# Optimization experiments

Measured on AMD Instinct MI355X. Metric: run time of the kernel, lower is better.

The kernel has to match this reference:

```python
import jax, jax.numpy as jnp
import numpy as np

B, S, E, H = 2, 2048, 1024, 16
D = E // H  # head_dim = 64
MASKED_BIAS = -10000.0


def setup_inputs() -> dict:
    key = jax.random.key(0)
    k1, k2, k3 = jax.random.split(key, 3)
    return {
        "hidden_states": jax.random.normal(k1, (B, S, E), dtype=jnp.float32),
        "w_attn": jax.random.normal(k2, (E, 3 * E), dtype=jnp.float32) * 0.02,
        "b_attn": jnp.zeros((3 * E,), dtype=jnp.float32),
        "w_proj": jax.random.normal(k3, (E, E), dtype=jnp.float32) * 0.02,
        "b_proj": jnp.zeros((E,), dtype=jnp.float32),
    }


def reference(hidden_states, w_attn, b_attn, w_proj, b_proj):
    # c_attn: [B,S,E] @ [E,3E] + bias
    qkv = hidden_states @ w_attn + b_attn
    q, k, v = jnp.split(qkv, 3, axis=-1)

    def split_heads(t):  # [B,S,E] -> [B,H,S,D]
        return t.reshape(B, S, H, D).transpose(0, 2, 1, 3)

    q, k, v = split_heads(q), split_heads(k), split_heads(v)

    # scores: [B,H,S,S], scaled by sqrt(head_dim)
    scores = jnp.einsum("bhqd,bhkd->bhqk", q, k) / jnp.float32(D) ** 0.5
    causal = jnp.tril(jnp.ones((S, S), dtype=bool))
    scores = jnp.where(causal, scores, jnp.float32(MASKED_BIAS))
    attn_weights = jax.nn.softmax(scores, axis=-1)
    # dropout p=0 (eval): identity
    attn_out = jnp.einsum("bhqk,bhkd->bhqd", attn_weights, v)
    # merge heads: [B,H,S,D] -> [B,S,E]
    attn_out = attn_out.transpose(0, 2, 1, 3).reshape(B, S, E)
    attn_out = attn_out @ w_proj + b_proj
    return attn_out, attn_weights
```

## Files before the change

kernel.cpp:

```cpp
#include <hip/hip_runtime.h>


typedef unsigned short u16;
typedef __attribute__((ext_vector_type(8))) short bf16x8;
typedef __attribute__((ext_vector_type(4))) float f32x4;
typedef __attribute__((ext_vector_type(4))) unsigned short u16x4;

#define MFMA(a, b, c) __builtin_amdgcn_mfma_f32_16x16x32_bf16((a), (b), (c), 0, 0, 0)

typedef const __attribute__((address_space(1))) void* gas_t;
typedef __attribute__((address_space(3))) void* las_t;
__device__ __forceinline__ void async_copy16(const void* g, void* l) {
  __builtin_amdgcn_global_load_lds((gas_t)g, (las_t)l, 16, 0, 0);
}

__device__ __forceinline__ u16 f2bf(float f) {
  unsigned u = __builtin_bit_cast(unsigned, f);
  u += 0x7FFFu + ((u >> 16) & 1u);
  return (u16)(u >> 16);
}
__device__ __forceinline__ float E2(float x) { return __builtin_amdgcn_exp2f(x); }

#define QSCALE 0.18033688011112042f

__global__ __launch_bounds__(256) void k_cast(const float* __restrict__ in,
                                              u16* __restrict__ out, int n) {
  int i = (blockIdx.x * 256 + threadIdx.x) * 4;
  if (i + 3 < n) {
    float4 v = *(const float4*)(in + i);
    u16x4 o = { f2bf(v.x), f2bf(v.y), f2bf(v.z), f2bf(v.w) };
    *(u16x4*)(out + i) = o;
  }
}

__global__ __launch_bounds__(256) void k_transpose_cast(const float* __restrict__ in,
                                                        u16* __restrict__ out,
                                                        int Kd, int Nd) {
  __shared__ float tile[64][65];
  int n0 = blockIdx.x * 64, k0 = blockIdx.y * 64;
  int t = threadIdx.x, col = t & 63, r4 = t >> 6;
#pragma unroll
  for (int ph = 0; ph < 16; ++ph) {
    int row = ph * 4 + r4;
    tile[row][col] = in[(size_t)(k0 + row) * Nd + n0 + col];
  }
  __syncthreads();
#pragma unroll
  for (int ph = 0; ph < 16; ++ph) {
    int row = ph * 4 + r4;
    out[(size_t)(n0 + row) * Kd + k0 + col] = f2bf(tile[col][row]);
  }
}

__global__ __launch_bounds__(256) void k_transpose_v(const u16* __restrict__ V,
                                                     u16* __restrict__ Vt) {
  __shared__ u16 tile[64][65];
  int bh = blockIdx.y, s0 = blockIdx.x * 64;
  int t = threadIdx.x, col = t & 63, r4 = t >> 6;
#pragma unroll
  for (int ph = 0; ph < 16; ++ph) {
    int row = ph * 4 + r4;
    tile[row][col] = V[((size_t)bh * 2048 + s0 + row) * 64 + col];
  }
  __syncthreads();
#pragma unroll
  for (int ph = 0; ph < 16; ++ph) {
    int row = ph * 4 + r4;
    Vt[((size_t)bh * 64 + row) * 2048 + s0 + col] = tile[col][row];
  }
}

#define GEMM_PROLOG()                                                          \
  __shared__ u16 As[128 * 32];                                                 \
  __shared__ u16 Bs[128 * 32];                                                 \
  int t = threadIdx.x;                                                         \
  int wave = t >> 6, lane = t & 63, quad = lane >> 4, l16 = lane & 15;         \
  int wm = wave >> 1, wn = wave & 1;                                           \
  int m0 = blockIdx.y * 128, n0 = blockIdx.x * 128;                            \
  int f1 = wave * 64 + lane, f2 = f1 + 256;                                    \
  const u16* gA1 = A + (size_t)(m0 + (f1 >> 2)) * 1024 + (f1 & 3) * 8;         \
  const u16* gA2 = A + (size_t)(m0 + (f2 >> 2)) * 1024 + (f2 & 3) * 8;         \
  const u16* gB1 = Bt + (size_t)(n0 + (f1 >> 2)) * 1024 + (f1 & 3) * 8;        \
  const u16* gB2 = Bt + (size_t)(n0 + (f2 >> 2)) * 1024 + (f2 & 3) * 8;        \
  u16* lA1 = As + wave * 512;                                                  \
  u16* lA2 = As + 2048 + wave * 512;                                           \
  u16* lB1 = Bs + wave * 512;                                                  \
  u16* lB2 = Bs + 2048 + wave * 512;                                           \
  f32x4 acc[4][4];                                                             \
  for (int i = 0; i < 4; ++i)                                                  \
    for (int j = 0; j < 4; ++j) acc[i][j] = (f32x4){0.f, 0.f, 0.f, 0.f};       \
  for (int k0 = 0; k0 < 1024; k0 += 32) {                                      \
    async_copy16(gA1 + k0, lA1);                                               \
    async_copy16(gA2 + k0, lA2);                                               \
    async_copy16(gB1 + k0, lB1);                                               \
    async_copy16(gB2 + k0, lB2);                                               \
    __syncthreads();                                                           \
    bf16x8 fa[4], fb[4];                                                       \
    _Pragma("unroll") for (int i = 0; i < 4; ++i)                              \
        fa[i] = *(const bf16x8*)(As + (wm * 64 + i * 16 + l16) * 32 + quad * 8);\
    _Pragma("unroll") for (int j = 0; j < 4; ++j)                              \
        fb[j] = *(const bf16x8*)(Bs + (wn * 64 + j * 16 + l16) * 32 + quad * 8);\
    _Pragma("unroll") for (int i = 0; i < 4; ++i)                              \
      _Pragma("unroll") for (int j = 0; j < 4; ++j)                            \
          acc[i][j] = MFMA(fa[i], fb[j], acc[i][j]);                           \
    __syncthreads();                                                           \
  }

__global__ __launch_bounds__(256) void k_gemm_qkv(const u16* __restrict__ A,
                                                  const u16* __restrict__ Bt,
                                                  const float* __restrict__ bias,
                                                  u16* __restrict__ Q,
                                                  u16* __restrict__ Kp,
                                                  u16* __restrict__ V) {
  GEMM_PROLOG()
#pragma unroll
  for (int j = 0; j < 4; ++j) {
    int n = n0 + wn * 64 + j * 16 + l16;
    float bv = bias[n];
    int which = n >> 10, e = n & 1023, h = e >> 6, d = e & 63;
#pragma unroll
    for (int i = 0; i < 4; ++i)
#pragma unroll
      for (int r = 0; r < 4; ++r) {
        int m = m0 + wm * 64 + i * 16 + quad * 4 + r;
        int b = m >> 11, s = m & 2047;
        float v = acc[i][j][r] + bv;
        size_t off = ((size_t)((b * 16 + h) * 2048 + s)) * 64 + d;
        if (which == 0)      Q[off]  = f2bf(v * QSCALE);
        else if (which == 1) Kp[off] = f2bf(v);
        else                 V[off]  = f2bf(v);
      }
  }
}

__global__ __launch_bounds__(256) void k_gemm_proj(const u16* __restrict__ A,
                                                   const u16* __restrict__ Bt,
                                                   const float* __restrict__ bias,
                                                   float* __restrict__ out) {
  GEMM_PROLOG()
#pragma unroll
  for (int j = 0; j < 4; ++j) {
    int n = n0 + wn * 64 + j * 16 + l16;
    float bv = bias[n];
#pragma unroll
    for (int i = 0; i < 4; ++i)
#pragma unroll
      for (int r = 0; r < 4; ++r) {
        int m = m0 + wm * 64 + i * 16 + quad * 4 + r;
        out[(size_t)m * 1024 + n] = acc[i][j][r] + bv;
      }
  }
}

__global__ __launch_bounds__(256, 4) void k_attn(const u16* __restrict__ Q,
                                                 const u16* __restrict__ Kp,
                                                 const u16* __restrict__ Vt,
                                                 u16* __restrict__ ctx,
                                                 float* __restrict__ Wout) {
  __shared__ float Pf[4][16 * 36];
  int t = threadIdx.x;
  int w = t >> 6, lane = t & 63, quad = lane >> 4, l16 = lane & 15;
  int id = blockIdx.x;
  int bh = id & 31;
  int ii = id >> 5, jj = ii & 7, ss = ii >> 3;
  int qt = (ss == 0) ? jj : (ss == 1) ? 15 - jj : (ss == 2) ? 16 + jj : 31 - jj;
  int q0 = qt * 64 + w * 16;

  const u16* qrow = Q + ((size_t)bh * 2048 + q0 + l16) * 64 + quad * 8;
  bf16x8 aq0 = *(const bf16x8*)(qrow);
  bf16x8 aq1 = *(const bf16x8*)(qrow + 32);

  const u16* kbase = Kp + (size_t)bh * 2048 * 64;
  int qmax = q0 + 15;

  float m0[4], l0[4], m1[4], l1[4];
#pragma unroll
  for (int r = 0; r < 4; ++r) { m0[r] = m1[r] = -1e30f; l0[r] = l1[r] = 0.f; }
  int nt = (q0 + 47) >> 5;

  const u16* kr0 = kbase + (size_t)l16 * 64 + quad * 8;
  bf16x8 nb00 = *(const bf16x8*)(kr0);
  bf16x8 nb01 = *(const bf16x8*)(kr0 + 32);
  bf16x8 nb10 = *(const bf16x8*)(kr0 + 1024);
  bf16x8 nb11 = *(const bf16x8*)(kr0 + 1024 + 32);
  for (int kt = 0; kt < nt; ++kt) {
    bf16x8 b00 = nb00, b01 = nb01, b10 = nb10, b11 = nb11;
    if (kt + 1 < nt) {
      const u16* kn = kbase + (size_t)((kt + 1) * 32 + l16) * 64 + quad * 8;
      nb00 = *(const bf16x8*)(kn);
      nb01 = *(const bf16x8*)(kn + 32);
      nb10 = *(const bf16x8*)(kn + 1024);
      nb11 = *(const bf16x8*)(kn + 1024 + 32);
    }
    f32x4 c0 = {0.f, 0.f, 0.f, 0.f}, c1 = c0;
    c0 = MFMA(aq0, b00, c0);
    c0 = MFMA(aq1, b01, c0);
    c1 = MFMA(aq0, b10, c1);
    c1 = MFMA(aq1, b11, c1);
    int col0 = kt * 32 + l16, col1 = col0 + 16;
#pragma unroll
    for (int r = 0; r < 4; ++r) {
      int q = q0 + quad * 4 + r;
      float v0 = (col0 <= q) ? c0[r] : -1e30f;
      float nm0 = fmaxf(m0[r], v0);
      l0[r] = l0[r] * E2(m0[r] - nm0) + E2(v0 - nm0);
      m0[r] = nm0;
      float v1 = (col1 <= q) ? c1[r] : -1e30f;
      float nm1 = fmaxf(m1[r], v1);
      l1[r] = l1[r] * E2(m1[r] - nm1) + E2(v1 - nm1);
      m1[r] = nm1;
    }
  }
  float m[4], l[4];
#pragma unroll
  for (int r = 0; r < 4; ++r) {
    float nm = fmaxf(m0[r], m1[r]);
    l[r] = l0[r] * E2(m0[r] - nm) + l1[r] * E2(m1[r] - nm);
    m[r] = nm;
  }
#pragma unroll
  for (int r = 0; r < 4; ++r) {
#pragma unroll
    for (int off = 1; off < 16; off <<= 1) {
      float om = __shfl_xor(m[r], off, 16);
      float ol = __shfl_xor(l[r], off, 16);
      float nm = fmaxf(m[r], om);
      l[r] = l[r] * E2(m[r] - nm) + ol * E2(om - nm);
      m[r] = nm;
    }
  }
  float rl[4];
#pragma unroll
  for (int r = 0; r < 4; ++r) rl[r] = 1.f / l[r];

  f32x4 oacc[4];
#pragma unroll
  for (int s4 = 0; s4 < 4; ++s4) oacc[s4] = (f32x4){0.f, 0.f, 0.f, 0.f};
  float* pf = &Pf[w][0];
  const u16* vtb = Vt + (size_t)bh * 64 * 2048;
  float* wrow = Wout + (size_t)bh * 2048 * 2048;
  int srow = lane >> 3, scol = (lane & 7) << 2;

  int na = qmax / 32 + 1;
  for (int kt2 = 0; kt2 < na; ++kt2) {
    int k0 = kt2 * 32;
    f32x4 cc[2] = {{0.f,0.f,0.f,0.f}, {0.f,0.f,0.f,0.f}};
    const u16* kr = kbase + (size_t)(k0 + l16) * 64 + quad * 8;
    bf16x8 b00 = *(const bf16x8*)(kr);
    bf16x8 b01 = *(const bf16x8*)(kr + 32);
    bf16x8 b10 = *(const bf16x8*)(kr + 1024);
    bf16x8 b11 = *(const bf16x8*)(kr + 1024 + 32);
    cc[0] = MFMA(aq0, b00, cc[0]);
    cc[0] = MFMA(aq1, b01, cc[0]);
    cc[1] = MFMA(aq0, b10, cc[1]);
    cc[1] = MFMA(aq1, b11, cc[1]);
#pragma unroll
    for (int sub = 0; sub < 2; ++sub) {
      int col = k0 + sub * 16 + l16;
#pragma unroll
      for (int r = 0; r < 4; ++r) {
        int q = q0 + quad * 4 + r;
        float p = (col <= q) ? E2(cc[sub][r] - m[r]) * rl[r] : 0.f;
        pf[(quad * 4 + r) * 36 + sub * 16 + l16] = p;
      }
    }
    f32x4 v0 = *(const f32x4*)(pf + srow * 36 + scol);
    f32x4 v1 = *(const f32x4*)(pf + (srow + 8) * 36 + scol);
    *(f32x4*)(wrow + (size_t)(q0 + srow) * 2048 + k0 + scol) = v0;
    *(f32x4*)(wrow + (size_t)(q0 + srow + 8) * 2048 + k0 + scol) = v1;
    f32x4 pa0 = *(const f32x4*)(pf + l16 * 36 + quad * 8);
    f32x4 pa1 = *(const f32x4*)(pf + l16 * 36 + quad * 8 + 4);
    bf16x8 pa;
#pragma unroll
    for (int e = 0; e < 4; ++e) {
      pa[e]     = (short)f2bf(pa0[e]);
      pa[e + 4] = (short)f2bf(pa1[e]);
    }
#pragma unroll
    for (int s4 = 0; s4 < 4; ++s4) {
      const u16* vr = vtb + (size_t)(s4 * 16 + l16) * 2048 + k0 + quad * 8;
      bf16x8 bv = *(const bf16x8*)(vr);
      oacc[s4] = MFMA(pa, bv, oacc[s4]);
    }
  }
  int zstart = na * 32;
  f32x4 z = {0.f, 0.f, 0.f, 0.f};
  for (int r = 0; r < 16; ++r) {
    float* rb = wrow + (size_t)(q0 + r) * 2048;
    for (int c = zstart + (lane << 2); c < 2048; c += 256)
      *(f32x4*)(rb + c) = z;
  }
  int b = bh >> 4, h = bh & 15;
#pragma unroll
  for (int s4 = 0; s4 < 4; ++s4)
#pragma unroll
    for (int r = 0; r < 4; ++r) {
      int q = q0 + quad * 4 + r;
      int d = s4 * 16 + l16;
      ctx[((size_t)(b * 2048 + q)) * 1024 + h * 64 + d] = f2bf(oacc[s4][r]);
    }
}

extern "C" void kernel_launch(void* const* d_in, const int* in_sizes, int n_in,
                              void* d_out, int out_size, void* d_ws, size_t ws_size,
                              hipStream_t stream) {
  const float* hs     = (const float*)d_in[0];
  const float* w_attn = (const float*)d_in[1];
  const float* b_attn = (const float*)d_in[2];
  const float* w_proj = (const float*)d_in[3];
  const float* b_proj = (const float*)d_in[4];

  char*  outc  = (char*)d_out;
  float* out_f = (float*)d_out;
  float* Wout  = out_f + 4194304;

  u16* qbuf = (u16*)outc;
  u16* kbuf = (u16*)(outc + 8388608);
  u16* hsb  = (u16*)(outc + 530579456);
  u16* wtA  = (u16*)(outc + 538968064);
  u16* vbuf = (u16*)(outc + 545259520);

  char* ws  = (char*)d_ws;
  u16*  vt  = (u16*)ws;
  u16*  ctx = (u16*)(ws + 8388608);
  u16*  wtP = (u16*)(ws + 16777216);

  k_cast<<<4096, 256, 0, stream>>>(hs, hsb, 4194304);
  k_transpose_cast<<<dim3(48, 16), 256, 0, stream>>>(w_attn, wtA, 1024, 3072);
  k_transpose_cast<<<dim3(16, 16), 256, 0, stream>>>(w_proj, wtP, 1024, 1024);
  k_gemm_qkv<<<dim3(24, 32), 256, 0, stream>>>(hsb, wtA, b_attn, qbuf, kbuf, vbuf);
  k_transpose_v<<<dim3(32, 32), 256, 0, stream>>>(vbuf, vt);
  k_attn<<<1024, 256, 0, stream>>>(qbuf, kbuf, vt, ctx, Wout);
  k_gemm_proj<<<dim3(8, 32), 256, 0, stream>>>(ctx, wtP, b_proj, out_f);
}
```

Baseline: 798.0 us.

## Narrow proj GEMM tiles, use single-exp online softmax, prefetch V loads

Three separate changes. The projection GEMM now has its own 128x64 tile kernel and a 16x32 grid, giving more blocks to fill the CUs. The online max/sum update in the attention stats pass now computes one exp2 per element instead of two, using exp2 of the negative absolute difference and a select. The V fragment loads in the second attention pass are issued before the QK MFMAs so their latency overlaps the softmax work, at the cost of more live registers.

Measured after the change: 778.7 us. 2.4% less time.

```diff
diff --git a/kernel.cpp b/kernel.cpp
--- a/kernel.cpp
+++ b/kernel.cpp
@@ -137,10 +137,43 @@
                                                    const u16* __restrict__ Bt,
                                                    const float* __restrict__ bias,
                                                    float* __restrict__ out) {
-  GEMM_PROLOG()
-#pragma unroll
-  for (int j = 0; j < 4; ++j) {
-    int n = n0 + wn * 64 + j * 16 + l16;
+  __shared__ u16 As[128 * 32];
+  __shared__ u16 Bs[64 * 32];
+  int t = threadIdx.x;
+  int wave = t >> 6, lane = t & 63, quad = lane >> 4, l16 = lane & 15;
+  int wm = wave >> 1, wn = wave & 1;
+  int m0 = blockIdx.y * 128, n0 = blockIdx.x * 64;
+  int f1 = wave * 64 + lane, f2 = f1 + 256;
+  const u16* gA1 = A + (size_t)(m0 + (f1 >> 2)) * 1024 + (f1 & 3) * 8;
+  const u16* gA2 = A + (size_t)(m0 + (f2 >> 2)) * 1024 + (f2 & 3) * 8;
+  const u16* gB1 = Bt + (size_t)(n0 + (f1 >> 2)) * 1024 + (f1 & 3) * 8;
+  u16* lA1 = As + wave * 512;
+  u16* lA2 = As + 2048 + wave * 512;
+  u16* lB1 = Bs + wave * 512;
+  f32x4 acc[4][2];
+  for (int i = 0; i < 4; ++i)
+    for (int j = 0; j < 2; ++j) acc[i][j] = (f32x4){0.f, 0.f, 0.f, 0.f};
+  for (int k0 = 0; k0 < 1024; k0 += 32) {
+    async_copy16(gA1 + k0, lA1);
+    async_copy16(gA2 + k0, lA2);
+    async_copy16(gB1 + k0, lB1);
+    __syncthreads();
+    bf16x8 fa[4], fb[2];
+#pragma unroll
+    for (int i = 0; i < 4; ++i)
+      fa[i] = *(const bf16x8*)(As + (wm * 64 + i * 16 + l16) * 32 + quad * 8);
+#pragma unroll
+    for (int j = 0; j < 2; ++j)
+      fb[j] = *(const bf16x8*)(Bs + (wn * 32 + j * 16 + l16) * 32 + quad * 8);
+#pragma unroll
+    for (int i = 0; i < 4; ++i)
+#pragma unroll
+      for (int j = 0; j < 2; ++j) acc[i][j] = MFMA(fa[i], fb[j], acc[i][j]);
+    __syncthreads();
+  }
+#pragma unroll
+  for (int j = 0; j < 2; ++j) {
+    int n = n0 + wn * 32 + j * 16 + l16;
     float bv = bias[n];
 #pragma unroll
     for (int i = 0; i < 4; ++i)
@@ -202,13 +235,17 @@
     for (int r = 0; r < 4; ++r) {
       int q = q0 + quad * 4 + r;
       float v0 = (col0 <= q) ? c0[r] : -1e30f;
-      float nm0 = fmaxf(m0[r], v0);
-      l0[r] = l0[r] * E2(m0[r] - nm0) + E2(v0 - nm0);
-      m0[r] = nm0;
+      float d0 = v0 - m0[r];
+      float t0 = E2(-__builtin_fabsf(d0));
+      bool g0 = d0 > 0.f;
+      l0[r] = g0 ? __builtin_fmaf(l0[r], t0, 1.f) : (l0[r] + t0);
+      m0[r] = g0 ? v0 : m0[r];
       float v1 = (col1 <= q) ? c1[r] : -1e30f;
-      float nm1 = fmaxf(m1[r], v1);
-      l1[r] = l1[r] * E2(m1[r] - nm1) + E2(v1 - nm1);
-      m1[r] = nm1;
+      float d1 = v1 - m1[r];
+      float t1 = E2(-__builtin_fabsf(d1));
+      bool g1 = d1 > 0.f;
+      l1[r] = g1 ? __builtin_fmaf(l1[r], t1, 1.f) : (l1[r] + t1);
+      m1[r] = g1 ? v1 : m1[r];
     }
   }
   float m[4], l[4];
@@ -244,12 +281,16 @@
   int na = qmax / 32 + 1;
   for (int kt2 = 0; kt2 < na; ++kt2) {
     int k0 = kt2 * 32;
-    f32x4 cc[2] = {{0.f,0.f,0.f,0.f}, {0.f,0.f,0.f,0.f}};
     const u16* kr = kbase + (size_t)(k0 + l16) * 64 + quad * 8;
     bf16x8 b00 = *(const bf16x8*)(kr);
     bf16x8 b01 = *(const bf16x8*)(kr + 32);
     bf16x8 b10 = *(const bf16x8*)(kr + 1024);
     bf16x8 b11 = *(const bf16x8*)(kr + 1024 + 32);
+    bf16x8 bv[4];
+#pragma unroll
+    for (int s4 = 0; s4 < 4; ++s4)
+      bv[s4] = *(const bf16x8*)(vtb + (size_t)(s4 * 16 + l16) * 2048 + k0 + quad * 8);
+    f32x4 cc[2] = {{0.f,0.f,0.f,0.f}, {0.f,0.f,0.f,0.f}};
     cc[0] = MFMA(aq0, b00, cc[0]);
     cc[0] = MFMA(aq1, b01, cc[0]);
     cc[1] = MFMA(aq0, b10, cc[1]);
@@ -278,9 +319,7 @@
     }
 #pragma unroll
     for (int s4 = 0; s4 < 4; ++s4) {
-      const u16* vr = vtb + (size_t)(s4 * 16 + l16) * 2048 + k0 + quad * 8;
-      bf16x8 bv = *(const bf16x8*)(vr);
-      oacc[s4] = MFMA(pa, bv, oacc[s4]);
+      oacc[s4] = MFMA(pa, bv[s4], oacc[s4]);
     }
   }
   int zstart = na * 32;
@@ -331,5 +370,5 @@
   k_gemm_qkv<<<dim3(24, 32), 256, 0, stream>>>(hsb, wtA, b_attn, qbuf, kbuf, vbuf);
   k_transpose_v<<<dim3(32, 32), 256, 0, stream>>>(vbuf, vt);
   k_attn<<<1024, 256, 0, stream>>>(qbuf, kbuf, vt, ctx, Wout);
-  k_gemm_proj<<<dim3(8, 32), 256, 0, stream>>>(ctx, wtP, b_proj, out_f);
-}
+  k_gemm_proj<<<dim3(16, 32), 256, 0, stream>>>(ctx, wtP, b_proj, out_f);
+}
```
